# Kernel tuning notes

Measured on AMD Instinct MI355X. Metric: run time of the kernel, lower is better.

Reference implementation:

```python
import jax, jax.numpy as jnp
import numpy as np

B, H, W, C = 16, 256, 256, 3
K_MAX = 64


def setup_inputs() -> dict:
    key = jax.random.key(0)
    k1, k2, k3 = jax.random.split(key, 3)
    images = jax.random.uniform(k1, (B, H, W, C), dtype=jnp.float32)
    palettes = jax.random.uniform(k2, (B, K_MAX, C), dtype=jnp.float32)
    # ragged palette sizes in [1, K_MAX]; entries >= size are padding
    palette_sizes = jax.random.randint(k3, (B,), 1, K_MAX + 1, dtype=jnp.int32)
    temperature = jnp.float32(1.0)
    return {"images": images, "palettes": palettes,
            "palette_sizes": palette_sizes, "temperature": temperature}


def reference(images, palettes, palette_sizes, temperature):
    # valid-entry mask emulating the ragged [B, (K), C] palette
    mask = jnp.arange(K_MAX)[None, :] < palette_sizes[:, None]          # [B, K]
    # per-pixel squared distance to each palette color: [B, H, W, K]
    diff = images[:, :, :, None, :] - palettes[:, None, None, :, :]
    distances = jnp.sum(diff * diff, axis=-1)
    logits = -distances / temperature
    # padded palette slots get -inf logits -> zero softmax weight,
    # exactly matching the ragged softmax over K_i entries
    logits = jnp.where(mask[:, None, None, :], logits, -jnp.inf)
    weights = jax.nn.softmax(logits, axis=-1)                            # [B, H, W, K]
    # softmax-weighted color blend (padded slots contribute 0)
    return jnp.einsum('bhwk,bkc->bhwc', weights, palettes)
```

## Files before the change

kernel.cpp:

```cpp
#include <hip/hip_runtime.h>


#define BATCH 16
#define HW 65536
#define KMAX 64
#define BLOCKS_PER_IMG 256
#define CF_ELEMS (BATCH * KMAX * 4)

__constant__ float cf_const[CF_ELEMS];

__global__ __launch_bounds__(64) void coef_kernel(
    const float* __restrict__ palettes,
    const float* __restrict__ temperature,
    float*       __restrict__ cf)
{
    const int b = blockIdx.x;
    const int k = threadIdx.x;
    const float scale = 1.4426950408889634f / temperature[0];

    const float pr = palettes[(b * KMAX + k) * 3 + 0];
    const float pg = palettes[(b * KMAX + k) * 3 + 1];
    const float pb = palettes[(b * KMAX + k) * 3 + 2];

    float* o = cf + ((b * KMAX + k) << 2);
    o[0] = 2.0f * pr * scale;
    o[1] = 2.0f * pg * scale;
    o[2] = 2.0f * pb * scale;
    o[3] = (-(pr * pr + pg * pg + pb * pb) - 3.0f) * scale;
}

__global__ __launch_bounds__(256) void palette_blend_kernel(
    const float* __restrict__ images,
    const int*   __restrict__ palette_sizes,
    const float* __restrict__ temperature,
    float*       __restrict__ out)
{
    const int b   = blockIdx.x >> 8;
    const int pix = ((blockIdx.x & (BLOCKS_PER_IMG - 1)) << 8) + threadIdx.x;
    const int K   = palette_sizes[b];

    const long base = (long)b * (HW * 3) + (long)pix * 3;
    const float x0 = images[base + 0];
    const float x1 = images[base + 1];
    const float x2 = images[base + 2];

    const int cbase = (b * KMAX) << 2;

    float s = 0.0f, o0 = 0.0f, o1 = 0.0f, o2 = 0.0f;
    #pragma unroll 4
    for (int k = 0; k < K; ++k) {
        const float a0 = cf_const[cbase + (k << 2) + 0];
        const float a1 = cf_const[cbase + (k << 2) + 1];
        const float a2 = cf_const[cbase + (k << 2) + 2];
        const float c  = cf_const[cbase + (k << 2) + 3];
        const float l  = fmaf(a0, x0, fmaf(a1, x1, fmaf(a2, x2, c)));
        const float w  = exp2f(l);
        s  += w;
        o0 = fmaf(w, a0, o0);
        o1 = fmaf(w, a1, o1);
        o2 = fmaf(w, a2, o2);
    }

    const float scale = 1.4426950408889634f / temperature[0];
    const float inv   = 1.0f / (s * 2.0f * scale);
    out[base + 0] = o0 * inv;
    out[base + 1] = o1 * inv;
    out[base + 2] = o2 * inv;
}

extern "C" void kernel_launch(void* const* d_in, const int* in_sizes, int n_in,
                              void* d_out, int out_size, void* d_ws, size_t ws_size,
                              hipStream_t stream) {
    const float* images        = (const float*)d_in[0];
    const float* palettes      = (const float*)d_in[1];
    const int*   palette_sizes = (const int*)d_in[2];
    const float* temperature   = (const float*)d_in[3];
    float*       out           = (float*)d_out;
    float*       cf            = (float*)d_ws;

    void* sym = nullptr;
    (void)hipGetSymbolAddress(&sym, HIP_SYMBOL(cf_const));

    coef_kernel<<<dim3(BATCH), dim3(KMAX), 0, stream>>>(palettes, temperature, cf);
    (void)hipMemcpyAsync(sym, cf, CF_ELEMS * sizeof(float),
                         hipMemcpyDeviceToDevice, stream);
    palette_blend_kernel<<<dim3(BATCH * BLOCKS_PER_IMG), dim3(256), 0, stream>>>(
        images, palette_sizes, temperature, out);
}
```

Baseline: 85.70 us.

## Process four pixels per thread with float4 I/O and drop constant-memory copy

Each thread now handles four pixels, loading and storing them as three float4 vectors, and reuses each palette coefficient load across all four pixels. Coefficients are read as float4 from the workspace buffer (global/scalar loads) rather than copied into __constant__ memory, which removes the device-to-device memcpy from the launch sequence. The grid shrinks fourfold, which trades occupancy and parallelism for more ILP and fewer per-pixel loads.

After: 84.99 us. About the same (-0.8%).

```diff
diff --git a/kernel.cpp b/kernel.cpp
--- a/kernel.cpp
+++ b/kernel.cpp
@@ -4,15 +4,13 @@
 #define BATCH 16
 #define HW 65536
 #define KMAX 64
-#define BLOCKS_PER_IMG 256
-#define CF_ELEMS (BATCH * KMAX * 4)
-
-__constant__ float cf_const[CF_ELEMS];
+#define PX_PER_THREAD 4
+#define BLOCKS_PER_IMG 64
 
 __global__ __launch_bounds__(64) void coef_kernel(
     const float* __restrict__ palettes,
     const float* __restrict__ temperature,
-    float*       __restrict__ cf)
+    float4*      __restrict__ cf)
 {
     const int b = blockIdx.x;
     const int k = threadIdx.x;
@@ -22,50 +20,70 @@
     const float pg = palettes[(b * KMAX + k) * 3 + 1];
     const float pb = palettes[(b * KMAX + k) * 3 + 2];
 
-    float* o = cf + ((b * KMAX + k) << 2);
-    o[0] = 2.0f * pr * scale;
-    o[1] = 2.0f * pg * scale;
-    o[2] = 2.0f * pb * scale;
-    o[3] = (-(pr * pr + pg * pg + pb * pb) - 3.0f) * scale;
+    float4 q;
+    q.x = 2.0f * pr * scale;
+    q.y = 2.0f * pg * scale;
+    q.z = 2.0f * pb * scale;
+    q.w = (-(pr * pr + pg * pg + pb * pb) - 3.0f) * scale;
+    cf[b * KMAX + k] = q;
 }
 
 __global__ __launch_bounds__(256) void palette_blend_kernel(
     const float* __restrict__ images,
     const int*   __restrict__ palette_sizes,
     const float* __restrict__ temperature,
+    const float4* __restrict__ cf,
     float*       __restrict__ out)
 {
-    const int b   = blockIdx.x >> 8;
-    const int pix = ((blockIdx.x & (BLOCKS_PER_IMG - 1)) << 8) + threadIdx.x;
-    const int K   = palette_sizes[b];
+    const int b    = blockIdx.x >> 6;
+    const int blk  = blockIdx.x & (BLOCKS_PER_IMG - 1);
+    const int pix0 = (blk << 10) + (threadIdx.x << 2);
+    const int K    = palette_sizes[b];
 
-    const long base = (long)b * (HW * 3) + (long)pix * 3;
-    const float x0 = images[base + 0];
-    const float x1 = images[base + 1];
-    const float x2 = images[base + 2];
+    const long base = (long)b * (HW * 3) + (long)pix0 * 3;
+    const float4 v0 = *(const float4*)(images + base + 0);
+    const float4 v1 = *(const float4*)(images + base + 4);
+    const float4 v2 = *(const float4*)(images + base + 8);
 
-    const int cbase = (b * KMAX) << 2;
+    const float xA0 = v0.x, xA1 = v0.y, xA2 = v0.z;
+    const float xB0 = v0.w, xB1 = v1.x, xB2 = v1.y;
+    const float xC0 = v1.z, xC1 = v1.w, xC2 = v2.x;
+    const float xD0 = v2.y, xD1 = v2.z, xD2 = v2.w;
 
-    float s = 0.0f, o0 = 0.0f, o1 = 0.0f, o2 = 0.0f;
-    #pragma unroll 4
+    const float4* __restrict__ c4 = cf + b * KMAX;
+
+    float sA = 0.f, aA0 = 0.f, aA1 = 0.f, aA2 = 0.f;
+    float sB = 0.f, aB0 = 0.f, aB1 = 0.f, aB2 = 0.f;
+    float sC = 0.f, aC0 = 0.f, aC1 = 0.f, aC2 = 0.f;
+    float sD = 0.f, aD0 = 0.f, aD1 = 0.f, aD2 = 0.f;
+
+    #pragma unroll 2
     for (int k = 0; k < K; ++k) {
-        const float a0 = cf_const[cbase + (k << 2) + 0];
-        const float a1 = cf_const[cbase + (k << 2) + 1];
-        const float a2 = cf_const[cbase + (k << 2) + 2];
-        const float c  = cf_const[cbase + (k << 2) + 3];
-        const float l  = fmaf(a0, x0, fmaf(a1, x1, fmaf(a2, x2, c)));
-        const float w  = exp2f(l);
-        s  += w;
-        o0 = fmaf(w, a0, o0);
-        o1 = fmaf(w, a1, o1);
-        o2 = fmaf(w, a2, o2);
+        const float4 A = c4[k];
+        const float lA = fmaf(A.x, xA0, fmaf(A.y, xA1, fmaf(A.z, xA2, A.w)));
+        const float lB = fmaf(A.x, xB0, fmaf(A.y, xB1, fmaf(A.z, xB2, A.w)));
+        const float lC = fmaf(A.x, xC0, fmaf(A.y, xC1, fmaf(A.z, xC2, A.w)));
+        const float lD = fmaf(A.x, xD0, fmaf(A.y, xD1, fmaf(A.z, xD2, A.w)));
+        const float wA = exp2f(lA), wB = exp2f(lB), wC = exp2f(lC), wD = exp2f(lD);
+        sA += wA; aA0 = fmaf(wA, A.x, aA0); aA1 = fmaf(wA, A.y, aA1); aA2 = fmaf(wA, A.z, aA2);
+        sB += wB; aB0 = fmaf(wB, A.x, aB0); aB1 = fmaf(wB, A.y, aB1); aB2 = fmaf(wB, A.z, aB2);
+        sC += wC; aC0 = fmaf(wC, A.x, aC0); aC1 = fmaf(wC, A.y, aC1); aC2 = fmaf(wC, A.z, aC2);
+        sD += wD; aD0 = fmaf(wD, A.x, aD0); aD1 = fmaf(wD, A.y, aD1); aD2 = fmaf(wD, A.z, aD2);
     }
 
     const float scale = 1.4426950408889634f / temperature[0];
-    const float inv   = 1.0f / (s * 2.0f * scale);
-    out[base + 0] = o0 * inv;
-    out[base + 1] = o1 * inv;
-    out[base + 2] = o2 * inv;
+    const float h = 0.5f / scale;
+    const float iA = h / sA, iB = h / sB, iC = h / sC, iD = h / sD;
+
+    float4 o0, o1, o2;
+    o0.x = aA0 * iA; o0.y = aA1 * iA; o0.z = aA2 * iA;
+    o0.w = aB0 * iB; o1.x = aB1 * iB; o1.y = aB2 * iB;
+    o1.z = aC0 * iC; o1.w = aC1 * iC; o2.x = aC2 * iC;
+    o2.y = aD0 * iD; o2.z = aD1 * iD; o2.w = aD2 * iD;
+
+    *(float4*)(out + base + 0) = o0;
+    *(float4*)(out + base + 4) = o1;
+    *(float4*)(out + base + 8) = o2;
 }
 
 extern "C" void kernel_launch(void* const* d_in, const int* in_sizes, int n_in,
@@ -76,14 +94,9 @@
     const int*   palette_sizes = (const int*)d_in[2];
     const float* temperature   = (const float*)d_in[3];
     float*       out           = (float*)d_out;
-    float*       cf            = (float*)d_ws;
-
-    void* sym = nullptr;
-    (void)hipGetSymbolAddress(&sym, HIP_SYMBOL(cf_const));
+    float4*      cf            = (float4*)d_ws;
 
     coef_kernel<<<dim3(BATCH), dim3(KMAX), 0, stream>>>(palettes, temperature, cf);
-    (void)hipMemcpyAsync(sym, cf, CF_ELEMS * sizeof(float),
-                         hipMemcpyDeviceToDevice, stream);
     palette_blend_kernel<<<dim3(BATCH * BLOCKS_PER_IMG), dim3(256), 0, stream>>>(
-        images, palette_sizes, temperature, out);
+        images, palette_sizes, temperature, cf, out);
 }
```
